# Performance work log

Hardware: AMD Instinct MI355X
Metric: run time of the kernel (lower is better)

## Reference

```python
import jax, jax.numpy as jnp
import numpy as np
import math

N_SAMPLES = 16384
BATCH = 16384
EPS = 0.001


def setup_inputs() -> dict:
    key = jax.random.key(0)
    k1, k2, k3 = jax.random.split(key, 3)
    x = jax.random.normal(k1, (BATCH, 1), dtype=jnp.float32)
    # learned parameters (initialized as in the torch module, plus small noise
    # on pot/logprob so gradients/logsumexp are non-degenerate)
    pos = jnp.linspace(-1.0, 7.0, N_SAMPLES, dtype=jnp.float32)[:, None]  # [M, 1]
    logprob = jnp.full((N_SAMPLES,), -math.log(N_SAMPLES), dtype=jnp.float32) \
        + 0.01 * jax.random.normal(k2, (N_SAMPLES,), dtype=jnp.float32)
    pot = 0.1 * jax.random.normal(k3, (N_SAMPLES,), dtype=jnp.float32)
    return {"x": x, "pos": pos, "logprob": logprob, "pot": pot}


def reference(x, pos, logprob, pot):
    # normalized log-probabilities over the M support points
    lp = logprob - jax.nn.logsumexp(logprob)  # [M]
    # pairwise squared-distance / 2: [N, M]
    dist = ((x ** 2).sum(axis=1)[:, None]
            + (pos ** 2).sum(axis=1)[None, :]
            - 2.0 * x @ pos.T) / 2.0
    term = lp[None, :] + (pot[None, :] - dist) / EPS  # [N, M]
    # softmin: -eps * logsumexp over support dim
    return -EPS * jax.nn.logsumexp(term, axis=1)  # [N]
```

## Files before the change

kernel.cpp:

```cpp
#include <hip/hip_runtime.h>
#include <hip/hip_bf16.h>
#include <math.h>


#define M_SUPPORT 16384
#define N_BATCH   16384
#define EPS_V  0.001f
#define XB     8.0f
#define MARGIN 1e-5f

__global__ __launch_bounds__(64) void zero_cnt_kernel(int* __restrict__ cnt) {
    if (threadIdx.x == 0) cnt[0] = 0;
}

__global__ __launch_bounds__(256) void prune_kernel(
    const float* __restrict__ pos, const float* __restrict__ logprob,
    const float* __restrict__ pot, int* __restrict__ cnt,
    float2* __restrict__ list)
{
    __shared__ float lA[576];
    __shared__ float lD[576];
    __shared__ int   sf[4][64];
    const int t    = threadIdx.x;
    const int lm   = t & 63;
    const int sub  = t >> 6;
    const int base = blockIdx.x * 64 - 256;

    for (int i = t; i < 576; i += 256) {
        int idx = base + i;
        idx = idx < 0 ? 0 : (idx > M_SUPPORT - 1 ? M_SUPPORT - 1 : idx);
        const float p = pos[idx];
        lA[i] = p;
        lD[i] = pot[idx] + EPS_V * logprob[idx] - 0.5f * p * p;
    }
    __syncthreads();

    const float Am = lA[lm + 256];
    const float Dm = lD[lm + 256] + MARGIN;
    int dominated = 0;
    const int s0 = lm + sub * 128;
#pragma unroll 8
    for (int j = 0; j < 128; ++j) {
        const float a = lA[s0 + j];
        const float d = lD[s0 + j];
        dominated |= (d - XB * fabsf(a - Am) >= Dm) ? 1 : 0;
    }
    sf[sub][lm] = dominated;
    __syncthreads();

    if (sub == 0) {
        if (!(sf[0][lm] | sf[1][lm] | sf[2][lm] | sf[3][lm])) {
            const int slot = atomicAdd(cnt, 1);
            list[slot] = make_float2(Am, lD[lm + 256]);
        }
    }
}

__global__ __launch_bounds__(256) void eval_kernel(
    const float* __restrict__ xs, const int* __restrict__ cnt,
    const float2* __restrict__ list, float* __restrict__ out)
{
    const int t    = threadIdx.x;
    const int lane = t & 63;
    const int w    = t >> 6;
    const int base = blockIdx.x * 32;
    __shared__ float sm[4][32];

    const int n = *cnt;

    const float xv = xs[base + (lane & 31)];
    float xj[32];
#pragma unroll
    for (int j = 0; j < 32; ++j)
        xj[j] = __int_as_float(__builtin_amdgcn_readlane(__float_as_int(xv), j));

    float acc[32];
#pragma unroll
    for (int j = 0; j < 32; ++j) acc[j] = -INFINITY;

    for (int i = w * 64 + lane; i < n; i += 256) {
        const float2 ad = list[i];
#pragma unroll
        for (int j = 0; j < 32; ++j)
            acc[j] = fmaxf(acc[j], fmaf(ad.x, xj[j], ad.y));
    }

#pragma unroll
    for (int s5 = 0; s5 < 5; ++s5) {
        const int d = 1 << s5;
        const int h = 16 >> s5;
#pragma unroll
        for (int i = 0; i < h; ++i) {
            const float lo = acc[i], hi = acc[i + h];
            const float sent = (lane & d) ? lo : hi;
            const float got  = __shfl_xor(sent, d);
            acc[i] = (lane & d) ? fmaxf(hi, got) : fmaxf(lo, got);
        }
    }
    const float v = fmaxf(acc[0], __shfl_xor(acc[0], 32));
    const int j = (int)(__brev((unsigned)(lane & 31)) >> 27);
    if (lane < 32) sm[w][j] = v;
    __syncthreads();

    if (t < 32) {
        float M = sm[0][t];
#pragma unroll
        for (int k = 1; k < 4; ++k) M = fmaxf(M, sm[k][t]);
        const float x = xs[base + t];
        out[base + t] = 0.5f * x * x - M;
    }
}

extern "C" void kernel_launch(void* const* d_in, const int* in_sizes, int n_in,
                              void* d_out, int out_size, void* d_ws, size_t ws_size,
                              hipStream_t stream)
{
    const float* x       = (const float*)d_in[0];
    const float* pos     = (const float*)d_in[1];
    const float* logprob = (const float*)d_in[2];
    const float* pot     = (const float*)d_in[3];

    int*    cnt  = (int*)d_ws;
    float2* list = (float2*)((char*)d_ws + 16);
    float*  outp = (float*)d_out;

    hipLaunchKernelGGL(zero_cnt_kernel, dim3(1), dim3(64), 0, stream, cnt);
    hipLaunchKernelGGL(prune_kernel, dim3(M_SUPPORT / 64), dim3(256), 0, stream,
                       pos, logprob, pot, cnt, list);
    hipLaunchKernelGGL(eval_kernel, dim3(N_BATCH / 32), dim3(256), 0, stream,
                       x, cnt, list, outp);
}
```

Measured before the change: 70.10 us.

## Replace atomic compaction with per-block ballot lists and LDS-staged eval

The prune kernel now writes survivors into fixed per-block slots using a wavefront ballot and popcount instead of a global atomic counter, which removes the zero-counter launch. The dominance window shrinks from ±256 to ±128 neighbours. The eval kernel prefix-sums the per-block counts, gathers the compacted survivor list into LDS (up to a cap), and has each thread scan it for a single x, with no cross-lane max reduction. A narrower window may keep more survivors, and each block redoes the gather and scan. If the survivor count exceeds the cap, a slow fallback reads global memory directly.

```diff
diff --git a/kernel.cpp b/kernel.cpp
--- a/kernel.cpp
+++ b/kernel.cpp
@@ -8,25 +8,22 @@
 #define EPS_V  0.001f
 #define XB     8.0f
 #define MARGIN 1e-5f
-
-__global__ __launch_bounds__(64) void zero_cnt_kernel(int* __restrict__ cnt) {
-    if (threadIdx.x == 0) cnt[0] = 0;
-}
+#define CAP    8192
 
 __global__ __launch_bounds__(256) void prune_kernel(
     const float* __restrict__ pos, const float* __restrict__ logprob,
-    const float* __restrict__ pot, int* __restrict__ cnt,
+    const float* __restrict__ pot, int* __restrict__ cnts,
     float2* __restrict__ list)
 {
-    __shared__ float lA[576];
-    __shared__ float lD[576];
+    __shared__ float lA[320];
+    __shared__ float lD[320];
     __shared__ int   sf[4][64];
     const int t    = threadIdx.x;
     const int lm   = t & 63;
     const int sub  = t >> 6;
-    const int base = blockIdx.x * 64 - 256;
+    const int base = blockIdx.x * 64 - 128;
 
-    for (int i = t; i < 576; i += 256) {
+    for (int i = t; i < 320; i += 256) {
         int idx = base + i;
         idx = idx < 0 ? 0 : (idx > M_SUPPORT - 1 ? M_SUPPORT - 1 : idx);
         const float p = pos[idx];
@@ -35,12 +32,12 @@
     }
     __syncthreads();
 
-    const float Am = lA[lm + 256];
-    const float Dm = lD[lm + 256] + MARGIN;
+    const float Am = lA[lm + 128];
+    const float Dm = lD[lm + 128] + MARGIN;
     int dominated = 0;
-    const int s0 = lm + sub * 128;
+    const int s0 = sub * 80;
 #pragma unroll 8
-    for (int j = 0; j < 128; ++j) {
+    for (int j = 0; j < 80; ++j) {
         const float a = lA[s0 + j];
         const float d = lD[s0 + j];
         dominated |= (d - XB * fabsf(a - Am) >= Dm) ? 1 : 0;
@@ -48,67 +45,73 @@
     sf[sub][lm] = dominated;
     __syncthreads();
 
-    if (sub == 0) {
-        if (!(sf[0][lm] | sf[1][lm] | sf[2][lm] | sf[3][lm])) {
-            const int slot = atomicAdd(cnt, 1);
-            list[slot] = make_float2(Am, lD[lm + 256]);
+    if (t < 64) {
+        const int dom = sf[0][lm] | sf[1][lm] | sf[2][lm] | sf[3][lm];
+        const unsigned long long mask = __ballot(!dom);
+        if (!dom) {
+            const int slot = (int)__popcll(mask & ((1ull << lm) - 1ull));
+            list[blockIdx.x * 64 + slot] = make_float2(Am, lD[lm + 128]);
         }
+        if (lm == 0) cnts[blockIdx.x] = (int)__popcll(mask);
     }
 }
 
 __global__ __launch_bounds__(256) void eval_kernel(
-    const float* __restrict__ xs, const int* __restrict__ cnt,
+    const float* __restrict__ xs, const int* __restrict__ cnts,
     const float2* __restrict__ list, float* __restrict__ out)
 {
+    __shared__ __align__(16) float svraw[2 * CAP];
+    __shared__ int scnt[256];
+    __shared__ int wt[4];
+    float2* sv = (float2*)svraw;
+
     const int t    = threadIdx.x;
     const int lane = t & 63;
     const int w    = t >> 6;
-    const int base = blockIdx.x * 32;
-    __shared__ float sm[4][32];
 
-    const int n = *cnt;
+    const int c = cnts[t];
+    scnt[t] = c;
+    int sc = c;
+#pragma unroll
+    for (int d = 1; d < 64; d <<= 1) {
+        const int v = __shfl_up(sc, d);
+        if (lane >= d) sc += v;
+    }
+    if (lane == 63) wt[w] = sc;
+    __syncthreads();
+    int off = 0;
+    for (int k = 0; k < w; ++k) off += wt[k];
+    const int excl = off + sc - c;
+    for (int i = 0; i < c; ++i)
+        if (excl + i < CAP) sv[excl + i] = list[t * 64 + i];
+    const int n = wt[0] + wt[1] + wt[2] + wt[3];
+    __syncthreads();
 
-    const float xv = xs[base + (lane & 31)];
-    float xj[32];
-#pragma unroll
-    for (int j = 0; j < 32; ++j)
-        xj[j] = __int_as_float(__builtin_amdgcn_readlane(__float_as_int(xv), j));
+    const int nidx = blockIdx.x * 256 + t;
+    const float x = xs[nidx];
+    float acc = -INFINITY;
 
-    float acc[32];
-#pragma unroll
-    for (int j = 0; j < 32; ++j) acc[j] = -INFINITY;
-
-    for (int i = w * 64 + lane; i < n; i += 256) {
-        const float2 ad = list[i];
-#pragma unroll
-        for (int j = 0; j < 32; ++j)
-            acc[j] = fmaxf(acc[j], fmaf(ad.x, xj[j], ad.y));
+    if (n <= CAP) {
+        int i = 0;
+        for (; i + 2 <= n; i += 2) {
+            const float4 q = *(const float4*)&sv[i];
+            acc = fmaxf(fmaxf(acc, fmaf(q.x, x, q.y)), fmaf(q.z, x, q.w));
+        }
+        if (i < n) {
+            const float2 q = sv[i];
+            acc = fmaxf(acc, fmaf(q.x, x, q.y));
+        }
+    } else {
+        for (int b = 0; b < 256; ++b) {
+            const int nb = scnt[b];
+            for (int i = 0; i < nb; ++i) {
+                const float2 q = list[b * 64 + i];
+                acc = fmaxf(acc, fmaf(q.x, x, q.y));
+            }
+        }
     }
 
-#pragma unroll
-    for (int s5 = 0; s5 < 5; ++s5) {
-        const int d = 1 << s5;
-        const int h = 16 >> s5;
-#pragma unroll
-        for (int i = 0; i < h; ++i) {
-            const float lo = acc[i], hi = acc[i + h];
-            const float sent = (lane & d) ? lo : hi;
-            const float got  = __shfl_xor(sent, d);
-            acc[i] = (lane & d) ? fmaxf(hi, got) : fmaxf(lo, got);
-        }
-    }
-    const float v = fmaxf(acc[0], __shfl_xor(acc[0], 32));
-    const int j = (int)(__brev((unsigned)(lane & 31)) >> 27);
-    if (lane < 32) sm[w][j] = v;
-    __syncthreads();
-
-    if (t < 32) {
-        float M = sm[0][t];
-#pragma unroll
-        for (int k = 1; k < 4; ++k) M = fmaxf(M, sm[k][t]);
-        const float x = xs[base + t];
-        out[base + t] = 0.5f * x * x - M;
-    }
+    out[nidx] = 0.5f * x * x - acc;
 }
 
 extern "C" void kernel_launch(void* const* d_in, const int* in_sizes, int n_in,
@@ -120,13 +123,12 @@
     const float* logprob = (const float*)d_in[2];
     const float* pot     = (const float*)d_in[3];
 
-    int*    cnt  = (int*)d_ws;
-    float2* list = (float2*)((char*)d_ws + 16);
+    int*    cnts = (int*)d_ws;
+    float2* list = (float2*)((char*)d_ws + 1024);
     float*  outp = (float*)d_out;
 
-    hipLaunchKernelGGL(zero_cnt_kernel, dim3(1), dim3(64), 0, stream, cnt);
     hipLaunchKernelGGL(prune_kernel, dim3(M_SUPPORT / 64), dim3(256), 0, stream,
-                       pos, logprob, pot, cnt, list);
-    hipLaunchKernelGGL(eval_kernel, dim3(N_BATCH / 32), dim3(256), 0, stream,
-                       x, cnt, list, outp);
+                       pos, logprob, pot, cnts, list);
+    hipLaunchKernelGGL(eval_kernel, dim3(N_BATCH / 256), dim3(256), 0, stream,
+                       x, cnts, list, outp);
 }
```

After: 76.82 us. 1.1x slower.
